# Kernel optimization log

Measured on AMD Instinct MI355X. Metric: run time of the kernel, lower is better.

## Reference

```python
import jax, jax.numpy as jnp
import numpy as np

DIM_E, DIM_M, DIM_C = 1024, 64, 128
B, N = 4, 4096


def setup_inputs() -> dict:
    key = jax.random.key(0)
    ks = jax.random.split(key, 10)
    s = 1.0 / np.sqrt(DIM_E + DIM_C)
    return {
        "e": jax.random.normal(ks[0], (B, N, DIM_E), jnp.float32),
        "m": jax.random.normal(ks[1], (B, N, DIM_M), jnp.float32),
        "c": jax.random.normal(ks[2], (B, N, DIM_C), jnp.float32),
        "l": jax.random.uniform(ks[3], (B, N), jnp.float32),
        "Wq": jax.random.uniform(ks[4], (DIM_E + DIM_C, DIM_E), jnp.float32, -s, s),
        "bq": jax.random.uniform(ks[5], (DIM_E,), jnp.float32, -s, s),
        "Wk": jax.random.uniform(ks[6], (DIM_E + DIM_C, DIM_E), jnp.float32, -s, s),
        "bk": jax.random.uniform(ks[7], (DIM_E,), jnp.float32, -s, s),
        "Wv": jax.random.uniform(ks[8], (DIM_E + DIM_C, DIM_E), jnp.float32, -s, s),
        "bv": jax.random.uniform(ks[9], (DIM_E,), jnp.float32, -s, s),
    }


def reference(e, m, c, l, Wq, bq, Wk, bk, Wv, bv):
    x = jnp.concatenate([e, c], axis=-1)                       # [B,N,De+Dc]
    q = jnp.einsum('bnd,df->bnf', x, Wq) + bq                  # [B,N,De]
    k = jnp.einsum('bnd,df->bnf', x, Wk) + bk
    v = jnp.einsum('bnd,df->bnf', x, Wv) + bv
    scale = 1.0 / jnp.sqrt(jnp.asarray(q.shape[-1], q.dtype))
    attn_scores = jnp.einsum('bqd,bkd->bqk', q, k) * scale     # [B,N,N]
    membrane_mask = jnp.einsum('bqm,bkm->bqk', m, m)           # [B,N,N]
    lifespan_mask = l[:, :, None] * l[:, None, :]              # [B,N,N]
    adaptive_scores = attn_scores * membrane_mask * lifespan_mask
    attn_weights = jax.nn.softmax(adaptive_scores, axis=-1)
    h_tilde = jnp.einsum('bqk,bkd->bqd', attn_weights, v)      # [B,N,De]
    e_new = e + h_tilde
    return (e_new, h_tilde)
```

## Files before the change

kernel.cpp:

```cpp
#include <hip/hip_runtime.h>
#include <hip/hip_bf16.h>

#define DE 1024
#define DM 64
#define DC 128
#define DX 1152
#define NB 4
#define NN 4096
#define NT 16384

typedef _Float16 f16;
typedef _Float16 f16x4 __attribute__((ext_vector_type(4)));
typedef _Float16 f16x8 __attribute__((ext_vector_type(8)));
typedef float f32x4 __attribute__((ext_vector_type(4)));

__device__ __forceinline__ void g2l16(const void* g, void* l) {
  __builtin_amdgcn_global_load_lds(
      (const __attribute__((address_space(1))) unsigned int*)(unsigned long long)g,
      (__attribute__((address_space(3))) unsigned int*)(unsigned int)(unsigned long long)l,
      16, 0, 0);
}

#define MEMF() asm volatile("" ::: "memory")
#define BAR() { MEMF(); __builtin_amdgcn_s_barrier(); MEMF(); }

__global__ void build_x_kernel(const float* __restrict__ e, const float* __restrict__ c,
                               f16* __restrict__ Xb) {
  const int total = NT * DX / 4;
  for (int i = blockIdx.x * blockDim.x + threadIdx.x; i < total; i += gridDim.x * blockDim.x) {
    int idx = i * 4;
    int r = idx / DX, col = idx - r * DX;
    float4 v;
    if (col < DE) v = *(const float4*)(e + (long)r * DE + col);
    else          v = *(const float4*)(c + (long)r * DC + (col - DE));
    f16x4 o = { (f16)v.x, (f16)v.y, (f16)v.z, (f16)v.w };
    *(f16x4*)(Xb + (long)idx) = o;
  }
}

__global__ void conv_f16_kernel(const float* __restrict__ in, f16* __restrict__ out, int total4) {
  for (int i = blockIdx.x * blockDim.x + threadIdx.x; i < total4; i += gridDim.x * blockDim.x) {
    float4 v = *(const float4*)(in + (long)i * 4);
    f16x4 o = { (f16)v.x, (f16)v.y, (f16)v.z, (f16)v.w };
    *(f16x4*)(out + (long)i * 4) = o;
  }
}

__global__ void transpose_w_kernel(const float* __restrict__ in, f16* __restrict__ out) {
  __shared__ float tile[32][33];
  int c0 = blockIdx.x * 32, r0 = blockIdx.y * 32;
  int x = threadIdx.x, y = threadIdx.y;
#pragma unroll
  for (int i = 0; i < 4; ++i)
    tile[y + 8 * i][x] = in[(long)(r0 + y + 8 * i) * DE + (c0 + x)];
  __syncthreads();
#pragma unroll
  for (int i = 0; i < 4; ++i)
    out[(long)(c0 + y + 8 * i) * DX + (r0 + x)] = (f16)tile[x][y + 8 * i];
}

__device__ __forceinline__ void mm_loop(const f16* __restrict__ A, const f16* __restrict__ B,
                                        int lda, int ldb, int K,
                                        f16* lA, f16* lB, f32x4 (&acc)[4][4]) {
  const int t = threadIdx.x;
  const int lane = t & 63;
  const int wid = t >> 6;
  const int wr = (wid >> 1) * 64, wc = (wid & 1) * 64;
  const int fr = lane & 15, fq = lane >> 4;
  for (int k0 = 0; k0 < K; k0 += 32) {
    __syncthreads();
#pragma unroll
    for (int it = 0; it < 2; ++it) {
      int byteoff = it * 4096 + t * 16;
      int row = byteoff >> 6;
      int ke = (byteoff & 63) >> 1;
      g2l16(A + (long)row * lda + k0 + ke, lA + (byteoff >> 1));
      g2l16(B + (long)row * ldb + k0 + ke, lB + (byteoff >> 1));
    }
    __syncthreads();
    f16x8 af[4], bfr[4];
#pragma unroll
    for (int i = 0; i < 4; ++i) {
      af[i]  = *(const f16x8*)(lA + (wr + i * 16 + fr) * 32 + fq * 8);
      bfr[i] = *(const f16x8*)(lB + (wc + i * 16 + fr) * 32 + fq * 8);
    }
#pragma unroll
    for (int m = 0; m < 4; ++m)
#pragma unroll
      for (int n = 0; n < 4; ++n)
        acc[m][n] = __builtin_amdgcn_mfma_f32_16x16x32_f16(af[m], bfr[n], acc[m][n], 0, 0, 0);
  }
}

__global__ __launch_bounds__(256) void mask_kernel(
    const f16* __restrict__ mb, const float* __restrict__ l, f16* __restrict__ Pm) {
  __shared__ __attribute__((aligned(16))) f16 lA[128 * 32], lB[128 * 32];
  f32x4 acc[4][4];
#pragma unroll
  for (int m = 0; m < 4; ++m)
#pragma unroll
    for (int n = 0; n < 4; ++n) acc[m][n] = (f32x4){0.f, 0.f, 0.f, 0.f};
  const int b = blockIdx.z;
  const int row0 = blockIdx.x * 128, col0 = blockIdx.y * 128;
  mm_loop(mb + (long)(b * NN + row0) * DM, mb + (long)(b * NN + col0) * DM,
          DM, DM, DM, lA, lB, acc);
  const int lane = threadIdx.x & 63, wid = threadIdx.x >> 6;
  const int wr = (wid >> 1) * 64, wc = (wid & 1) * 64;
  const int fr = lane & 15, fq = lane >> 4;
  const float* lb = l + (long)b * NN;
  f16* out = Pm + (long)b * NN * NN;
#pragma unroll
  for (int n = 0; n < 4; ++n) {
    int col = col0 + wc + n * 16 + fr;
    float lc = lb[col] * 0.03125f;
#pragma unroll
    for (int m = 0; m < 4; ++m)
#pragma unroll
      for (int r = 0; r < 4; ++r) {
        int row = row0 + wr + m * 16 + fq * 4 + r;
        out[(long)row * NN + col] = (f16)(acc[m][n][r] * lc * lb[row]);
      }
  }
}

__device__ __forceinline__ void gemm8_core(
    const f16* __restrict__ A, long lda,
    const f16* __restrict__ B, long ldb,
    int NTt, char* ldsb, f32x4 (&acc)[8][4]) {
  const int tid = threadIdx.x;
  const int lane = tid & 63, wid = tid >> 6;
  const int wr = wid >> 2, wc = wid & 3;
  const int fr = lane & 15, fq = lane >> 4;
  const int cb0 = ((fq) ^ (fr & 7)) << 4;
  const int cb1 = ((4 | fq) ^ (fr & 7)) << 4;

  auto stageA = [&](int pc, int kt, int par) {
    char* base = ldsb + par * 32768;
    int k0 = kt * 64;
#pragma unroll
    for (int it = 0; it < 2; ++it) {
      int p = it * 8192 + tid * 16;
      int off = pc * 8192 + ((p >> 13) << 14) + (p & 8191);
      int sw = off ^ (((off >> 7) & 7) << 4);
      int row = sw >> 7;
      int colf = ((sw >> 4) & 7) << 3;
      g2l16(A + (long)row * lda + k0 + colf, base + off);
    }
  };
  auto stageB = [&](int pc, int kt, int par) {
    char* base = ldsb + 65536 + par * 32768;
    int k0 = kt * 64;
#pragma unroll
    for (int it = 0; it < 2; ++it) {
      int p = it * 8192 + tid * 16;
      int off = pc * 4096 + ((p >> 12) << 13) + (p & 4095);
      int sw = off ^ (((off >> 7) & 7) << 4);
      int row = sw >> 7;
      int colf = ((sw >> 4) & 7) << 3;
      g2l16(B + (long)row * ldb + k0 + colf, base + off);
    }
  };

  f16x8 af[4][2], bf0[2][2], bf1[2][2];
  auto rdA = [&](int mh, int par) {
    const char* base = ldsb + par * 32768;
#pragma unroll
    for (int i = 0; i < 4; ++i) {
      int row = wr * 128 + mh * 64 + i * 16 + fr;
      af[i][0] = *(const f16x8*)(const void*)(base + row * 128 + cb0);
      af[i][1] = *(const f16x8*)(const void*)(base + row * 128 + cb1);
    }
  };
  auto rdB = [&](f16x8 (&bf)[2][2], int nh, int par) {
    const char* base = ldsb + 65536 + par * 32768;
#pragma unroll
    for (int i = 0; i < 2; ++i) {
      int row = wc * 64 + nh * 32 + i * 16 + fr;
      bf[i][0] = *(const f16x8*)(const void*)(base + row * 128 + cb0);
      bf[i][1] = *(const f16x8*)(const void*)(base + row * 128 + cb1);
    }
  };
  auto mma = [&](f16x8 (&bf)[2][2], int mo, int no) {
    __builtin_amdgcn_s_setprio(1);
#pragma unroll
    for (int m = 0; m < 4; ++m)
#pragma unroll
      for (int n = 0; n < 2; ++n)
#pragma unroll
        for (int k = 0; k < 2; ++k)
          acc[mo + m][no + n] =
              __builtin_amdgcn_mfma_f32_16x16x32_f16(af[m][k], bf[n][k], acc[mo + m][no + n], 0, 0, 0);
    __builtin_amdgcn_s_setprio(0);
  };

  MEMF();
  stageA(0, 0, 0); stageB(0, 0, 0); stageA(1, 0, 0); stageB(1, 0, 0);
  stageA(0, 1, 1); stageB(0, 1, 1); stageA(1, 1, 1);
  asm volatile("s_waitcnt vmcnt(6)" ::: "memory");
  BAR();

  for (int t = 0; t < NTt; t += 2) {
#pragma unroll
    for (int half = 0; half < 2; ++half) {
      const int tt = t + half;
      const int par = half, npar = half ^ 1;
      rdA(0, par); rdB(bf0, 0, par);
      if (tt + 1 < NTt) stageB(1, tt + 1, npar);
      BAR();
      mma(bf0, 0, 0);
      BAR();
      rdB(bf1, 1, par);
      if (tt + 2 < NTt) stageA(0, tt + 2, par);
      BAR();
      mma(bf1, 0, 2);
      BAR();
      rdA(1, par);
      if (tt + 2 < NTt) stageB(0, tt + 2, par);
      BAR();
      mma(bf1, 4, 2);
      BAR();
      if (tt + 2 < NTt) stageA(1, tt + 2, par);
      BAR();
      mma(bf0, 4, 0);
      if (tt + 1 < NTt) {
        if (tt + 1 == NTt - 1) { asm volatile("s_waitcnt vmcnt(0)" ::: "memory"); }
        else                   { asm volatile("s_waitcnt vmcnt(6)" ::: "memory"); }
      }
      BAR();
    }
  }
  MEMF();
}

__device__ __forceinline__ void swz_grid(int& bx, int& by, int& bz) {
  int nx = gridDim.x, ny = gridDim.y;
  int flat = blockIdx.x + nx * (blockIdx.y + ny * blockIdx.z);
  int total = nx * ny * gridDim.z;
  int cpx = total >> 3;
  flat = (flat & 7) * cpx + (flat >> 3);
  bx = flat % nx; int r = flat / nx;
  by = r % ny; bz = r / ny;
}

#define ACC_INIT()                                                  \
  f32x4 acc[8][4];                                                  \
  _Pragma("unroll") for (int m_ = 0; m_ < 8; ++m_)                  \
  _Pragma("unroll") for (int n_ = 0; n_ < 4; ++n_)                  \
      acc[m_][n_] = (f32x4){0.f, 0.f, 0.f, 0.f};

#define EPI8_IDX()                                                  \
  const int lane = threadIdx.x & 63, wid = threadIdx.x >> 6;        \
  const int wr = wid >> 2, wc = wid & 3;                            \
  const int fr = lane & 15, fq = lane >> 4;

__global__ __launch_bounds__(512, 2) void qk8_kernel(
    const f16* __restrict__ Xb, const f16* __restrict__ Wt,
    const float* __restrict__ bq, const float* __restrict__ bk,
    f16* __restrict__ qb, f16* __restrict__ kb) {
  __shared__ __attribute__((aligned(128))) char ldsb[131072];
  int bx, by, bz; swz_grid(bx, by, bz);
  const int row0 = bx * 256, col0 = by * 256;
  ACC_INIT();
  gemm8_core(Xb + (long)row0 * DX, DX, Wt + (long)col0 * DX, DX, DX / 64, ldsb, acc);
  EPI8_IDX();
  const bool isq = col0 < DE;
  const float* bvec = isq ? bq : bk;
  f16* ob = isq ? qb : kb;
  const int cbase = (isq ? col0 : col0 - DE) + wc * 64;
  const int rbase = row0 + wr * 128;
#pragma unroll
  for (int n = 0; n < 4; ++n) {
    int col = cbase + n * 16 + fr;
    float bb = bvec[col];
#pragma unroll
    for (int m = 0; m < 8; ++m)
#pragma unroll
      for (int j = 0; j < 4; ++j) {
        int row = rbase + m * 16 + fq * 4 + j;
        ob[(long)row * DE + col] = (f16)(acc[m][n][j] + bb);
      }
  }
}

__global__ __launch_bounds__(512, 2) void vt8_kernel(
    const f16* __restrict__ WtV, const f16* __restrict__ Xb,
    const float* __restrict__ bv, f16* __restrict__ Vt) {
  __shared__ __attribute__((aligned(128))) char ldsb[131072];
  int bx, by, bz; swz_grid(bx, by, bz);
  const int row0 = bx * 256, col0 = by * 256;
  ACC_INIT();
  gemm8_core(WtV + (long)row0 * DX, DX, Xb + (long)col0 * DX, DX, DX / 64, ldsb, acc);
  EPI8_IDX();
  const int cbase = col0 + wc * 64;
  const int rbase = row0 + wr * 128;
#pragma unroll
  for (int n = 0; n < 4; ++n) {
    int col = cbase + n * 16 + fr;
#pragma unroll
    for (int m = 0; m < 8; ++m)
#pragma unroll
      for (int j = 0; j < 4; ++j) {
        int row = rbase + m * 16 + fq * 4 + j;
        Vt[(long)row * NT + col] = (f16)(acc[m][n][j] + bv[row]);
      }
  }
}

__global__ __launch_bounds__(512, 2) void sc8_kernel(
    const f16* __restrict__ qb_, const f16* __restrict__ kb_, float* __restrict__ S) {
  __shared__ __attribute__((aligned(128))) char ldsb[131072];
  int bx, by, bz; swz_grid(bx, by, bz);
  const int row0 = bx * 256, col0 = by * 256;
  ACC_INIT();
  gemm8_core(qb_ + (long)row0 * DE, DE, kb_ + (long)col0 * DE, DE, DE / 64, ldsb, acc);
  EPI8_IDX();
  const int cbase = col0 + wc * 64;
  const int rbase = row0 + wr * 128;
#pragma unroll
  for (int n = 0; n < 4; ++n) {
    int col = cbase + n * 16 + fr;
#pragma unroll
    for (int m = 0; m < 8; ++m)
#pragma unroll
      for (int j = 0; j < 4; ++j) {
        int row = rbase + m * 16 + fq * 4 + j;
        S[(long)row * NN + col] = acc[m][n][j];
      }
  }
}

__global__ __launch_bounds__(512, 2) void pv8_kernel(
    const f16* __restrict__ P, const f16* __restrict__ Vt,
    const float* __restrict__ e, float* __restrict__ outE, float* __restrict__ outH) {
  __shared__ __attribute__((aligned(128))) char ldsb[131072];
  int bx, by, bz; swz_grid(bx, by, bz);
  const int b = bz;
  const int row0 = bx * 256, col0 = by * 256;
  ACC_INIT();
  gemm8_core(P + (long)b * NN * NN + (long)row0 * NN, NN,
             Vt + (long)col0 * NT + (long)b * NN, NT, NN / 64, ldsb, acc);
  EPI8_IDX();
  const int cbase = col0 + wc * 64;
  const int rbase = row0 + wr * 128;
#pragma unroll
  for (int n = 0; n < 4; ++n) {
    int col = cbase + n * 16 + fr;
#pragma unroll
    for (int m = 0; m < 8; ++m)
#pragma unroll
      for (int j = 0; j < 4; ++j) {
        int row = rbase + m * 16 + fq * 4 + j;
        long idx = ((long)b * NN + row) * DE + col;
        float h = acc[m][n][j];
        outE[idx] = e[idx] + h;
        outH[idx] = h;
      }
  }
}

__global__ __launch_bounds__(256) void softmax_kernel(const float* __restrict__ S,
                                                      const f16* __restrict__ Pm,
                                                      f16* __restrict__ P) {
  __shared__ float red[8];
  const long row = blockIdx.x;
  const float* s = S + row * NN;
  const f16* pmr = Pm + row * NN;
  const int t = threadIdx.x;
  float4 v[4];
  float mx = -3.0e38f;
#pragma unroll
  for (int i = 0; i < 4; ++i) {
    v[i] = *(const float4*)(s + t * 4 + i * 1024);
    f16x4 m4 = *(const f16x4*)(pmr + t * 4 + i * 1024);
    v[i].x *= (float)m4[0]; v[i].y *= (float)m4[1];
    v[i].z *= (float)m4[2]; v[i].w *= (float)m4[3];
    mx = fmaxf(mx, fmaxf(fmaxf(v[i].x, v[i].y), fmaxf(v[i].z, v[i].w)));
  }
#pragma unroll
  for (int o = 32; o; o >>= 1) mx = fmaxf(mx, __shfl_xor(mx, o));
  if ((t & 63) == 0) red[t >> 6] = mx;
  __syncthreads();
  mx = fmaxf(fmaxf(red[0], red[1]), fmaxf(red[2], red[3]));
  float sum = 0.f;
#pragma unroll
  for (int i = 0; i < 4; ++i) {
    v[i].x = __expf(v[i].x - mx); v[i].y = __expf(v[i].y - mx);
    v[i].z = __expf(v[i].z - mx); v[i].w = __expf(v[i].w - mx);
    sum += v[i].x + v[i].y + v[i].z + v[i].w;
  }
#pragma unroll
  for (int o = 32; o; o >>= 1) sum += __shfl_xor(sum, o);
  if ((t & 63) == 0) red[4 + (t >> 6)] = sum;
  __syncthreads();
  float inv = 1.f / (red[4] + red[5] + red[6] + red[7]);
  f16* p = P + row * NN;
#pragma unroll
  for (int i = 0; i < 4; ++i) {
    f16x4 o4 = { (f16)(v[i].x * inv), (f16)(v[i].y * inv),
                 (f16)(v[i].z * inv), (f16)(v[i].w * inv) };
    *(f16x4*)(p + t * 4 + i * 1024) = o4;
  }
}

extern "C" void kernel_launch(void* const* d_in, const int* in_sizes, int n_in,
                              void* d_out, int out_size, void* d_ws, size_t ws_size,
                              hipStream_t stream) {
  const float* e  = (const float*)d_in[0];
  const float* m  = (const float*)d_in[1];
  const float* c  = (const float*)d_in[2];
  const float* l  = (const float*)d_in[3];
  const float* Wq = (const float*)d_in[4];
  const float* bq = (const float*)d_in[5];
  const float* Wk = (const float*)d_in[6];
  const float* bk = (const float*)d_in[7];
  const float* Wv = (const float*)d_in[8];
  const float* bv = (const float*)d_in[9];
  float* outE = (float*)d_out;
  float* outH = outE + (long)NT * DE;

  char* ws = (char*)d_ws;
  size_t off = 0;
  auto alloc = [&](size_t bytes) {
    char* p = ws + off;
    off += (bytes + 255) & ~(size_t)255;
    return p;
  };
  f16* Xb    = (f16*)alloc((size_t)NT * DX * 2);
  f16* WtQK  = (f16*)alloc((size_t)2048 * DX * 2);
  f16* WtV   = (f16*)alloc((size_t)DE * DX * 2);
  f16* qb    = (f16*)alloc((size_t)NT * DE * 2);
  f16* kb    = (f16*)alloc((size_t)NT * DE * 2);
  f16* Vt    = (f16*)alloc((size_t)DE * NT * 2);
  f16* mb    = (f16*)alloc((size_t)NT * DM * 2);
  float* S   = (float*)alloc((size_t)NN * NN * 4);
  f16* P     = (f16*)alloc((size_t)NB * NN * NN * 2);
  if (off > ws_size) return;

  build_x_kernel<<<2048, 256, 0, stream>>>(e, c, Xb);
  conv_f16_kernel<<<512, 256, 0, stream>>>(m, mb, NT * DM / 4);
  transpose_w_kernel<<<dim3(32, 36), dim3(32, 8), 0, stream>>>(Wq, WtQK);
  transpose_w_kernel<<<dim3(32, 36), dim3(32, 8), 0, stream>>>(Wk, WtQK + (size_t)DE * DX);
  transpose_w_kernel<<<dim3(32, 36), dim3(32, 8), 0, stream>>>(Wv, WtV);
  mask_kernel<<<dim3(32, 32, NB), 256, 0, stream>>>(mb, l, P);
  qk8_kernel<<<dim3(64, 8), 512, 0, stream>>>(Xb, WtQK, bq, bk, qb, kb);
  vt8_kernel<<<dim3(4, 64), 512, 0, stream>>>(WtV, Xb, bv, Vt);
  for (int b = 0; b < NB; ++b) {
    sc8_kernel<<<dim3(16, 16), 512, 0, stream>>>(
        qb + (size_t)b * NN * DE, kb + (size_t)b * NN * DE, S);
    softmax_kernel<<<NN, 256, 0, stream>>>(S, P + (size_t)b * NN * NN, P + (size_t)b * NN * NN);
  }
  pv8_kernel<<<dim3(16, 4, NB), 512, 0, stream>>>(P, Vt, e, outE, outH);
}
```

Baseline: 676.5 us.

## Restructure GEMM main loop to overlap LDS fragment reads with MFMA

Double-buffers the A fragments (af_a/af_b) and moves the first fragment reads of the next K-tile ahead of the loop. LDS reads and global-to-LDS staging now sit next to the MFMA blocks, and the barriers per half-iteration drop from eight to four. The aim is to hide LDS latency and cut barrier stalls, at the cost of extra VGPRs for the second A fragment set and a modified vmcnt accounting. The K-outer MFMA loop order also changes how the accumulator dependency chains interleave.

After: 1.210 ms. 78.8% more time.

```diff
diff --git a/kernel.cpp b/kernel.cpp
--- a/kernel.cpp
+++ b/kernel.cpp
@@ -161,8 +161,8 @@
     }
   };
 
-  f16x8 af[4][2], bf0[2][2], bf1[2][2];
-  auto rdA = [&](int mh, int par) {
+  f16x8 af_a[4][2], af_b[4][2], bf0[2][2], bf1[2][2];
+  auto rdA = [&](f16x8 (&af)[4][2], int mh, int par) {
     const char* base = ldsb + par * 32768;
 #pragma unroll
     for (int i = 0; i < 4; ++i) {
@@ -180,14 +180,14 @@
       bf[i][1] = *(const f16x8*)(const void*)(base + row * 128 + cb1);
     }
   };
-  auto mma = [&](f16x8 (&bf)[2][2], int mo, int no) {
+  auto mma = [&](f16x8 (&af)[4][2], f16x8 (&bf)[2][2], int mo, int no) {
     __builtin_amdgcn_s_setprio(1);
 #pragma unroll
-    for (int m = 0; m < 4; ++m)
-#pragma unroll
-      for (int n = 0; n < 2; ++n)
-#pragma unroll
-        for (int k = 0; k < 2; ++k)
+    for (int k = 0; k < 2; ++k)
+#pragma unroll
+      for (int m = 0; m < 4; ++m)
+#pragma unroll
+        for (int n = 0; n < 2; ++n)
           acc[mo + m][no + n] =
               __builtin_amdgcn_mfma_f32_16x16x32_f16(af[m][k], bf[n][k], acc[mo + m][no + n], 0, 0, 0);
     __builtin_amdgcn_s_setprio(0);
@@ -195,37 +195,33 @@
 
   MEMF();
   stageA(0, 0, 0); stageB(0, 0, 0); stageA(1, 0, 0); stageB(1, 0, 0);
-  stageA(0, 1, 1); stageB(0, 1, 1); stageA(1, 1, 1);
-  asm volatile("s_waitcnt vmcnt(6)" ::: "memory");
+  stageA(0, 1, 1); stageB(0, 1, 1); stageA(1, 1, 1); stageB(1, 1, 1);
+  asm volatile("s_waitcnt vmcnt(8)" ::: "memory");
   BAR();
+  rdA(af_a, 0, 0); rdB(bf0, 0, 0);
 
   for (int t = 0; t < NTt; t += 2) {
 #pragma unroll
     for (int half = 0; half < 2; ++half) {
       const int tt = t + half;
       const int par = half, npar = half ^ 1;
-      rdA(0, par); rdB(bf0, 0, par);
-      if (tt + 1 < NTt) stageB(1, tt + 1, npar);
+      mma(af_a, bf0, 0, 0);
+      rdB(bf1, 1, par);
       BAR();
-      mma(bf0, 0, 0);
+      if (tt + 2 < NTt) stageA(0, tt + 2, par);
+      mma(af_a, bf1, 0, 2);
+      rdA(af_b, 1, par);
       BAR();
-      rdB(bf1, 1, par);
-      if (tt + 2 < NTt) stageA(0, tt + 2, par);
+      if (tt + 2 < NTt) stageB(0, tt + 2, par);
+      mma(af_b, bf1, 4, 2);
+      if (tt + 1 < NTt) {
+        if (tt + 2 < NTt) { asm volatile("s_waitcnt vmcnt(4)" ::: "memory"); }
+        else              { asm volatile("s_waitcnt vmcnt(0)" ::: "memory"); }
+      }
       BAR();
-      mma(bf1, 0, 2);
-      BAR();
-      rdA(1, par);
-      if (tt + 2 < NTt) stageB(0, tt + 2, par);
-      BAR();
-      mma(bf1, 4, 2);
-      BAR();
-      if (tt + 2 < NTt) stageA(1, tt + 2, par);
-      BAR();
-      mma(bf0, 4, 0);
-      if (tt + 1 < NTt) {
-        if (tt + 1 == NTt - 1) { asm volatile("s_waitcnt vmcnt(0)" ::: "memory"); }
-        else                   { asm volatile("s_waitcnt vmcnt(6)" ::: "memory"); }
-      }
+      if (tt + 2 < NTt) { stageA(1, tt + 2, par); stageB(1, tt + 2, par); }
+      mma(af_b, bf0, 4, 0);
+      if (tt + 1 < NTt) { rdA(af_a, 0, npar); rdB(bf0, 0, npar); }
       BAR();
     }
   }
```

## Restructure GEMM pipeline barriers with sched_barrier and regroup B-tile staging

Applied to the files above, without the earlier changes.

Replaces the compiler memory fences around s_barrier with sched_barrier(0) fences and moves the vmcnt waits into a wrapper that also blocks reordering. The staging of the second B half-tile now happens together with the A half for tile tt+2 instead of one tile ahead, so each stage issues matching loads. The wait count changes to vmcnt(8) and the waits move before the last MMA block. The MFMA loop is also reordered to put k outermost. The aim is tighter control over instruction scheduling and fewer pipeline stalls, with a risk of hazards in the LDS reuse timing or less latency hiding for the B loads.

Result: no change. 679.8 us (+0.5%).

```diff
diff --git a/kernel.cpp b/kernel.cpp
--- a/kernel.cpp
+++ b/kernel.cpp
@@ -21,8 +21,11 @@
       16, 0, 0);
 }
 
-#define MEMF() asm volatile("" ::: "memory")
-#define BAR() { MEMF(); __builtin_amdgcn_s_barrier(); MEMF(); }
+#define SBAR() do { __builtin_amdgcn_sched_barrier(0);                 \
+                    __builtin_amdgcn_s_barrier();                      \
+                    __builtin_amdgcn_sched_barrier(0); } while (0)
+#define VMWAIT(n) do { asm volatile("s_waitcnt vmcnt(" #n ")");        \
+                       __builtin_amdgcn_sched_barrier(0); } while (0)
 
 __global__ void build_x_kernel(const float* __restrict__ e, const float* __restrict__ c,
                                f16* __restrict__ Xb) {
@@ -183,53 +186,51 @@
   auto mma = [&](f16x8 (&bf)[2][2], int mo, int no) {
     __builtin_amdgcn_s_setprio(1);
 #pragma unroll
-    for (int m = 0; m < 4; ++m)
-#pragma unroll
-      for (int n = 0; n < 2; ++n)
-#pragma unroll
-        for (int k = 0; k < 2; ++k)
+    for (int k = 0; k < 2; ++k)
+#pragma unroll
+      for (int m = 0; m < 4; ++m)
+#pragma unroll
+        for (int n = 0; n < 2; ++n)
           acc[mo + m][no + n] =
               __builtin_amdgcn_mfma_f32_16x16x32_f16(af[m][k], bf[n][k], acc[mo + m][no + n], 0, 0, 0);
     __builtin_amdgcn_s_setprio(0);
   };
 
-  MEMF();
   stageA(0, 0, 0); stageB(0, 0, 0); stageA(1, 0, 0); stageB(1, 0, 0);
-  stageA(0, 1, 1); stageB(0, 1, 1); stageA(1, 1, 1);
-  asm volatile("s_waitcnt vmcnt(6)" ::: "memory");
-  BAR();
+  stageA(0, 1, 1); stageB(0, 1, 1); stageA(1, 1, 1); stageB(1, 1, 1);
+  VMWAIT(8);
+  SBAR();
 
   for (int t = 0; t < NTt; t += 2) {
 #pragma unroll
     for (int half = 0; half < 2; ++half) {
       const int tt = t + half;
-      const int par = half, npar = half ^ 1;
+      const int par = half;
       rdA(0, par); rdB(bf0, 0, par);
-      if (tt + 1 < NTt) stageB(1, tt + 1, npar);
-      BAR();
+      SBAR();
       mma(bf0, 0, 0);
-      BAR();
+      SBAR();
       rdB(bf1, 1, par);
       if (tt + 2 < NTt) stageA(0, tt + 2, par);
-      BAR();
+      SBAR();
       mma(bf1, 0, 2);
-      BAR();
+      SBAR();
       rdA(1, par);
       if (tt + 2 < NTt) stageB(0, tt + 2, par);
-      BAR();
+      SBAR();
       mma(bf1, 4, 2);
-      BAR();
-      if (tt + 2 < NTt) stageA(1, tt + 2, par);
-      BAR();
+      SBAR();
+      if (tt + 2 < NTt) {
+        stageA(1, tt + 2, par); stageB(1, tt + 2, par);
+        VMWAIT(8);
+      } else if (tt + 1 < NTt) {
+        VMWAIT(0);
+      }
+      SBAR();
       mma(bf0, 4, 0);
-      if (tt + 1 < NTt) {
-        if (tt + 1 == NTt - 1) { asm volatile("s_waitcnt vmcnt(0)" ::: "memory"); }
-        else                   { asm volatile("s_waitcnt vmcnt(6)" ::: "memory"); }
-      }
-      BAR();
-    }
-  }
-  MEMF();
+      SBAR();
+    }
+  }
 }
 
 __device__ __forceinline__ void swz_grid(int& bx, int& by, int& bz) {
```
